# Kernel optimization log

Hardware: AMD Instinct MI355X
Metric: run time of the kernel (lower is better)

The kernel has to match this reference:

```python
import jax, jax.numpy as jnp
import numpy as np
from jax import lax

N_NEURONS = 128
BATCH = 2048
SEQ = 128
INFTY = 1e8


def setup_inputs() -> dict:
    key = jax.random.key(0)
    ks = jax.random.split(key, 10)
    n = N_NEURONS
    lim = 1.0 / np.sqrt(n)  # torch LSTMCell default init scale
    return {
        "enc_outputs": jax.random.normal(ks[0], (BATCH, SEQ, n), jnp.float32),
        "h0": jax.random.normal(ks[1], (BATCH, n), jnp.float32),
        "c0": jax.random.normal(ks[2], (BATCH, n), jnp.float32),
        "dec_first_input": jnp.zeros((1, n), jnp.float32),
        "W_ref": jax.random.normal(ks[3], (1, n, n), jnp.float32),
        "W_out": jax.random.normal(ks[4], (n, n), jnp.float32),
        "v": jax.random.normal(ks[5], (n,), jnp.float32),
        "W_ih": jax.random.uniform(ks[6], (4 * n, n), jnp.float32, -lim, lim),
        "W_hh": jax.random.uniform(ks[7], (4 * n, n), jnp.float32, -lim, lim),
        "b_ih": jax.random.uniform(ks[8], (4 * n,), jnp.float32, -lim, lim),
        "b_hh": jax.random.uniform(ks[9], (4 * n,), jnp.float32, -lim, lim),
    }


def _decode(enc_outputs, h0, c0, dec_first_input, W_ref, W_out, v, W_ih, W_hh, b_ih, b_hh):
    B, S, n = enc_outputs.shape
    # step-invariant pointer projection of encoder outputs (the conv1d term)
    enc_term = jnp.einsum("bsn,mn->bsm", enc_outputs, W_ref[0])  # [B,S,n]
    batch_idx = jnp.arange(B)
    keys = jax.random.split(jax.random.key(1234), S)
    inp0 = jnp.broadcast_to(dec_first_input, (B, n))
    mask0 = jnp.zeros((B, S), enc_outputs.dtype)

    def step(carry, key):
        h, c, mask, inp = carry
        # LSTMCell: gate order i, f, g, o (torch convention)
        gates = inp @ W_ih.T + b_ih + h @ W_hh.T + b_hh  # [B,4n]
        i_g, f_g, g_g, o_g = jnp.split(gates, 4, axis=1)
        c = jax.nn.sigmoid(f_g) * c + jax.nn.sigmoid(i_g) * jnp.tanh(g_g)
        h = jax.nn.sigmoid(o_g) * jnp.tanh(c)
        # pointer attention scores
        dec_term = (h @ W_out)[:, None, :]  # [B,1,n]
        scores = jnp.sum(v * jnp.tanh(enc_term + dec_term), axis=-1)  # [B,S]
        masked = scores - INFTY * mask
        loc = jax.random.categorical(key, masked)  # [B] int, non-differentiable sample
        logp = jnp.take_along_axis(jax.nn.log_softmax(masked, axis=1), loc[:, None], axis=1)[:, 0]
        mask = mask.at[batch_idx, loc].set(1.0)
        inp = enc_outputs[batch_idx, loc, :]  # gather next decoder input
        return (h, c, mask, inp), (loc, logp)

    _, (locs, logps) = lax.scan(step, (h0, c0, mask0, inp0), keys)
    locs = locs.T  # [B,S]
    tour = jnp.concatenate([locs, locs[:, :1]], axis=1)  # append first location
    log_prob = jnp.sum(logps, axis=0)  # [B]
    return log_prob, tour


def reference(enc_outputs, h0, c0, dec_first_input, W_ref, W_out, v, W_ih, W_hh, b_ih, b_hh):
    return _decode(enc_outputs, h0, c0, dec_first_input, W_ref, W_out, v, W_ih, W_hh, b_ih, b_hh)
```

## Files before the change

### kernel.cpp

```cpp
#include <hip/hip_runtime.h>
#include <cstdint>
#include <cstddef>

#pragma clang fp contract(off)

#define PRNG_PARTITIONABLE 1

#define INFTY_F 1.0e8f
#define TINY_F 1.17549435e-38f

__device__ __forceinline__ float fdiv_rn(float n, float q) {
  float y0 = __builtin_amdgcn_rcpf(q);
  float y  = fmaf(fmaf(-q, y0, 1.0f), y0, y0);
  float r0 = n * y;
  float e0 = fmaf(-q, r0, n);
  float r1 = fmaf(e0, y, r0);
  float e1 = fmaf(-q, r1, n);
  return fmaf(e1, y, r1);
}

__device__ __forceinline__ void tf2x32(uint32_t k0, uint32_t k1, uint32_t x0, uint32_t x1,
                                       uint32_t& o0, uint32_t& o1) {
  uint32_t ks2 = k0 ^ k1 ^ 0x1BD11BDAu;
  uint32_t v0 = x0 + k0, v1 = x1 + k1;
#define TF_R(r) { v0 += v1; v1 = (v1 << (r)) | (v1 >> (32 - (r))); v1 ^= v0; }
  TF_R(13) TF_R(15) TF_R(26) TF_R(6)
  v0 += k1;  v1 += ks2 + 1u;
  TF_R(17) TF_R(29) TF_R(16) TF_R(24)
  v0 += ks2; v1 += k0 + 2u;
  TF_R(13) TF_R(15) TF_R(26) TF_R(6)
  v0 += k0;  v1 += k1 + 3u;
  TF_R(17) TF_R(29) TF_R(16) TF_R(24)
  v0 += k1;  v1 += ks2 + 4u;
  TF_R(13) TF_R(15) TF_R(26) TF_R(6)
  v0 += ks2; v1 += k0 + 5u;
#undef TF_R
  o0 = v0; o1 = v1;
}

__device__ __forceinline__ uint32_t random_bits32(uint32_t k0, uint32_t k1, uint32_t j) {
#if PRNG_PARTITIONABLE
  uint32_t o0, o1;
  tf2x32(k0, k1, 0u, j, o0, o1);
  return o0 ^ o1;
#else
  uint32_t o0, o1;
  if (j < 131072u) { tf2x32(k0, k1, j, j + 131072u, o0, o1); return o0; }
  else             { tf2x32(k0, k1, j - 131072u, j, o0, o1); return o1; }
#endif
}

__device__ __forceinline__ float xla_tanhf(float x) {
  float xc = fminf(fmaxf(x, -9.0f), 9.0f);
  float x2 = xc * xc;
  float p = -2.76076847742355e-16f;
  p = (p * x2) + 2.00018790482477e-13f;
  p = (p * x2) + -8.60467152213735e-11f;
  p = (p * x2) + 5.12229709037114e-08f;
  p = (p * x2) + 1.48572235717979e-05f;
  p = (p * x2) + 6.37261928875436e-04f;
  p = (p * x2) + 4.89352455891786e-03f;
  float num = xc * p;
  float q = 1.19825839466702e-06f;
  q = (q * x2) + 1.18534705686654e-04f;
  q = (q * x2) + 2.26843463243900e-03f;
  q = (q * x2) + 4.89352518554385e-03f;
  float r = fdiv_rn(num, q);
  return (fabsf(x) < 0.0004f) ? x : r;
}

__device__ __forceinline__ void xla_tanh2(float xa, float xb, float& ra, float& rb) {
  float xca = fminf(fmaxf(xa, -9.0f), 9.0f);
  float xcb = fminf(fmaxf(xb, -9.0f), 9.0f);
  float x2a = xca * xca, x2b = xcb * xcb;
  float pa = -2.76076847742355e-16f, pb = -2.76076847742355e-16f;
  pa = (pa * x2a) + 2.00018790482477e-13f;  pb = (pb * x2b) + 2.00018790482477e-13f;
  pa = (pa * x2a) + -8.60467152213735e-11f; pb = (pb * x2b) + -8.60467152213735e-11f;
  pa = (pa * x2a) + 5.12229709037114e-08f;  pb = (pb * x2b) + 5.12229709037114e-08f;
  pa = (pa * x2a) + 1.48572235717979e-05f;  pb = (pb * x2b) + 1.48572235717979e-05f;
  pa = (pa * x2a) + 6.37261928875436e-04f;  pb = (pb * x2b) + 6.37261928875436e-04f;
  pa = (pa * x2a) + 4.89352455891786e-03f;  pb = (pb * x2b) + 4.89352455891786e-03f;
  float na = xca * pa, nb = xcb * pb;
  float qa = 1.19825839466702e-06f, qb = 1.19825839466702e-06f;
  qa = (qa * x2a) + 1.18534705686654e-04f; qb = (qb * x2b) + 1.18534705686654e-04f;
  qa = (qa * x2a) + 2.26843463243900e-03f; qb = (qb * x2b) + 2.26843463243900e-03f;
  qa = (qa * x2a) + 4.89352518554385e-03f; qb = (qb * x2b) + 4.89352518554385e-03f;
  float da = fdiv_rn(na, qa), db = fdiv_rn(nb, qb);
  ra = (fabsf(xa) < 0.0004f) ? xa : da;
  rb = (fabsf(xb) < 0.0004f) ? xb : db;
}

__device__ __forceinline__ float xla_expf(float x) {
  x = fminf(x, 88.3762626647950f);
  x = fmaxf(x, -88.3762626647949f);
  float m = floorf((x * 1.44269504088896341f) + 0.5f);
  float r = x - (m * 0.693359375f);
  r = r - (m * -2.12194440e-4f);
  float r2 = r * r;
  float y = 1.9875691500E-4f;
  y = (y * r) + 1.3981999507E-3f;
  y = (y * r) + 8.3334519073E-3f;
  y = (y * r) + 4.1665795894E-2f;
  y = (y * r) + 1.6666665459E-1f;
  y = (y * r) + 5.0000001201E-1f;
  y = (y * r2) + r;
  y = y + 1.0f;
  int mi = (int)m;
  float s = __uint_as_float((uint32_t)((mi + 127) << 23));
  return y * s;
}

__device__ __forceinline__ float xla_sigmoidf(float x) {
  return 1.0f / (1.0f + xla_expf(-x));
}

__device__ __forceinline__ float xla_logf(float x) {
  uint32_t b = __float_as_uint(x);
  float e = (float)((int)(b >> 23) - 126);
  float m = __uint_as_float((b & 0x007fffffu) | 0x3f000000u);
  bool mlt = (m < 0.707106781186547524f);
  float tmp = mlt ? m : 0.0f;
  e = e - (mlt ? 1.0f : 0.0f);
  float xx = (m - 1.0f) + tmp;
  float z = xx * xx;
  float y = 7.0376836292E-2f;
  y = (y * xx) + -1.1514610310E-1f;
  y = (y * xx) + 1.1676998740E-1f;
  y = (y * xx) + -1.2420140846E-1f;
  y = (y * xx) + 1.4249322787E-1f;
  y = (y * xx) + -1.6668057665E-1f;
  y = (y * xx) + 2.0000714765E-1f;
  y = (y * xx) + -2.4999993993E-1f;
  y = (y * xx) + 3.3333331174E-1f;
  y = y * xx;
  y = y * z;
  y = y + (e * -2.12194440e-4f);
  y = y - (z * 0.5f);
  float res = xx + y;
  res = res + (e * 0.693359375f);
  return res;
}

__device__ __forceinline__ float gumbel_from_bits(uint32_t bits) {
  float f = __uint_as_float((bits >> 9) | 0x3f800000u) - 1.0f;
  float u = (f * 1.0f) + TINY_F;
  u = fmaxf(TINY_F, u);
  return -xla_logf(-xla_logf(u));
}

__global__ void k_keys(uint32_t* __restrict__ keys) {
  int t = threadIdx.x;
  if (t >= 128) return;
#if PRNG_PARTITIONABLE
  uint32_t o0, o1;
  tf2x32(0u, 1234u, 0u, (uint32_t)t, o0, o1);
  keys[2 * t] = o0; keys[2 * t + 1] = o1;
#else
  uint32_t o0, o1, a, bb;
  if (t < 64) {
    tf2x32(0u, 1234u, (uint32_t)(2 * t),     (uint32_t)(128 + 2 * t), o0, o1); a  = o0;
    tf2x32(0u, 1234u, (uint32_t)(2 * t + 1), (uint32_t)(129 + 2 * t), o0, o1); bb = o0;
  } else {
    tf2x32(0u, 1234u, (uint32_t)(2 * t - 128), (uint32_t)(2 * t),     o0, o1); a  = o1;
    tf2x32(0u, 1234u, (uint32_t)(2 * t - 127), (uint32_t)(2 * t + 1), o0, o1); bb = o1;
  }
  keys[2 * t] = a; keys[2 * t + 1] = bb;
#endif
}

__global__ void k_trans(const float* __restrict__ Wih, const float* __restrict__ Whh,
                        float* __restrict__ WihT, float* __restrict__ WhhT) {
  int idx = blockIdx.x * blockDim.x + threadIdx.x;
  if (idx < 65536) {
    int r = idx >> 7, k = idx & 127;
    WihT[k * 512 + r] = Wih[idx];
    WhhT[k * 512 + r] = Whh[idx];
  }
}

__global__ __launch_bounds__(128) void k_encT(const float* __restrict__ enc,
                                              const float* __restrict__ Wref,
                                              float* __restrict__ encT) {
  __shared__ float el[64 * 132];
  __shared__ float ot[64 * 129];
  int tid = threadIdx.x;
  int b  = blockIdx.x >> 1;
  int sh = blockIdx.x & 1;
  const float* eb = enc + (size_t)b * 16384 + (size_t)sh * 8192;
  for (int i = tid; i < 8192; i += 128) {
    int s = i >> 7, n = i & 127;
    el[s * 132 + n] = eb[i];
  }
  __syncthreads();
  int sl = tid & 63;
  int mh = tid >> 6;
  for (int ml = 0; ml < 64; ++ml) {
    int m = mh * 64 + ml;
    const float4* wr = (const float4*)(Wref + m * 128);
    float acc = 0.0f;
#pragma unroll 8
    for (int q = 0; q < 32; ++q) {
      float4 w4 = wr[q];
      float4 e4 = *(const float4*)&el[sl * 132 + 4 * q];
      acc = fmaf(e4.x, w4.x, acc); acc = fmaf(e4.y, w4.y, acc);
      acc = fmaf(e4.z, w4.z, acc); acc = fmaf(e4.w, w4.w, acc);
    }
    ot[sl * 129 + m] = acc;
  }
  __syncthreads();
  float* op = encT + (size_t)b * 16384 + (size_t)(sh * 64) * 128;
  for (int i = tid; i < 8192; i += 128)
    op[i] = ot[(i >> 7) * 129 + (i & 127)];
}

__global__ __launch_bounds__(512, 4) void k_main(
    const float* __restrict__ enc, const float* __restrict__ h0,
    const float* __restrict__ c0, const float* __restrict__ dec_first,
    const float* __restrict__ W_out, const float* __restrict__ v,
    const float* __restrict__ b_ih, const float* __restrict__ b_hh,
    const float* __restrict__ WihT, const float* __restrict__ WhhT,
    const float* __restrict__ encT, const uint32_t* __restrict__ keys,
    float* __restrict__ out) {
  __shared__ float xI_s[128][8];
  __shared__ float c_s[4][128];
  __shared__ float gates_s[4][512];
  __shared__ float2 vdec2_s[4][128];
  __shared__ float bih_s[512];
  __shared__ float bhh_s[512];
  __shared__ float v_s[128];
  __shared__ uint32_t keys_s[256];
  __shared__ int cu_s[4][128];
  __shared__ int pos_s[4][128];
  __shared__ float val_s[512];
  __shared__ float msk_s[512];
  __shared__ int   sc_s[512];
  __shared__ int   loc_s[4];

  const int tid  = threadIdx.x;
  const int lane = tid & 63;
  const int w    = tid >> 6;
  const int g4   = w >> 1;
  const int half = w & 1;
  const int s4   = half * 64 + lane;
  const int bbase = blockIdx.x * 4;
  const int b4   = bbase + g4;

  bih_s[tid] = b_ih[tid];
  bhh_s[tid] = b_hh[tid];
  if (tid < 256) keys_s[tid] = keys[tid];
  if (tid < 128) v_s[tid] = v[tid];
  {
    int g = tid >> 7, j = tid & 127;
    xI_s[j][g]     = dec_first[j];
    xI_s[j][4 + g] = h0[(size_t)(bbase + g) * 128 + j];
    c_s[g][j] = c0[(size_t)(bbase + g) * 128 + j];
    cu_s[g][j] = j;
    pos_s[g][j] = j;
  }
  float logp_sum = 0.0f;
  float* tour = out + 2048;
  __syncthreads();

  for (int step = 0; step < 128; ++step) {
    {
      const int r = tid;
      float aA0 = 0.0f, aA1 = 0.0f, aA2 = 0.0f, aA3 = 0.0f;
      float aB0 = 0.0f, aB1 = 0.0f, aB2 = 0.0f, aB3 = 0.0f;
      const float* pih = WihT + r;
      const float* phh = WhhT + r;
#pragma unroll 8
      for (int k = 0; k < 128; ++k) {
        float4 xi = *(const float4*)&xI_s[k][0];
        float4 xh = *(const float4*)&xI_s[k][4];
        float wih = pih[k * 512], whh = phh[k * 512];
        aA0 = fmaf(xi.x, wih, aA0);
        aA1 = fmaf(xi.y, wih, aA1);
        aA2 = fmaf(xi.z, wih, aA2);
        aA3 = fmaf(xi.w, wih, aA3);
        aB0 = fmaf(xh.x, whh, aB0);
        aB1 = fmaf(xh.y, whh, aB1);
        aB2 = fmaf(xh.z, whh, aB2);
        aB3 = fmaf(xh.w, whh, aB3);
      }
      float b1 = bih_s[r], b2 = bhh_s[r];
      gates_s[0][r] = (((aA0 + b1) + aB0) + b2);
      gates_s[1][r] = (((aA1 + b1) + aB1) + b2);
      gates_s[2][r] = (((aA2 + b1) + aB2) + b2);
      gates_s[3][r] = (((aA3 + b1) + aB3) + b2);
    }
    __syncthreads();

    {
      int g = tid >> 7, j = tid & 127;
      float gi = gates_s[g][j], gf = gates_s[g][128 + j];
      float gg = gates_s[g][256 + j], go = gates_s[g][384 + j];
      float si = xla_sigmoidf(gi), sf = xla_sigmoidf(gf), so = xla_sigmoidf(go);
      float gt = xla_tanhf(gg);
      float cold = c_s[g][j];
      float cn = (sf * cold) + (si * gt);
      c_s[g][j] = cn;
      xI_s[j][4 + g] = so * xla_tanhf(cn);
    }
    __syncthreads();

    {
      int g = tid >> 7, m = tid & 127;
      float acc = 0.0f;
      const float* wo = W_out + m;
#pragma unroll 8
      for (int k = 0; k < 128; ++k)
        acc = fmaf(xI_s[k][4 + g], wo[k * 128], acc);
      vdec2_s[g][m] = make_float2(v_s[m], acc);
    }
    __syncthreads();

    const int u = 128 - step;
    {
      const int q = tid;
      float masked = -INFTY_F, val = -INFTY_F;
      int sc = 0x7fffffff;
      if (q < 4 * u) {
        int bq = (q >= u) + (q >= 2 * u) + (q >= 3 * u);
        int e  = q - bq * u;
        sc = cu_s[bq][e];
        const int bb = bbase + bq;
        uint32_t kk0 = keys_s[2 * step], kk1 = keys_s[2 * step + 1];
        uint32_t j0 = (uint32_t)bb * 128u + (uint32_t)sc;
        float gmb = gumbel_from_bits(random_bits32(kk0, kk1, j0));
        const float* ep = encT + ((size_t)bb * 128 + (size_t)sc) * 128;
        float acc = 0.0f;
#pragma unroll 8
        for (int m4 = 0; m4 < 32; ++m4) {
          float4 e4 = *(const float4*)&ep[4 * m4];
          float4 vd01 = *(const float4*)&vdec2_s[bq][4 * m4];
          float4 vd23 = *(const float4*)&vdec2_s[bq][4 * m4 + 2];
          float t0, t1, t2, t3;
          xla_tanh2(e4.x + vd01.y, e4.y + vd01.w, t0, t1);
          xla_tanh2(e4.z + vd23.y, e4.w + vd23.w, t2, t3);
          acc = acc + (vd01.x * t0);
          acc = acc + (vd01.z * t1);
          acc = acc + (vd23.x * t2);
          acc = acc + (vd23.z * t3);
        }
        masked = acc;
        val = gmb + masked;
      }
      val_s[q] = val;
      msk_s[q] = masked;
      sc_s[q]  = sc;
    }
    __syncthreads();

    if (w < 4) {
      const int g = w;
      const int base = g * u;
      float vaA = -INFTY_F, mkA = -INFTY_F;
      float vaB = -INFTY_F, mkB = -INFTY_F;
      int iaA = 0x7fffffff, iaB = 0x7fffffff;
      if (lane < u)      { vaA = val_s[base + lane];      iaA = sc_s[base + lane];      mkA = msk_s[base + lane]; }
      if (lane + 64 < u) { vaB = val_s[base + lane + 64]; iaB = sc_s[base + lane + 64]; mkB = msk_s[base + lane + 64]; }
      float va = vaA; int ia = iaA;
      if (vaB > va || (vaB == va && iaB < ia)) { va = vaB; ia = iaB; }
      float mx = fmaxf(mkA, mkB);
      float se = 0.0f;
#pragma unroll
      for (int off = 32; off > 0; off >>= 1) {
        float vo = __shfl_xor(va, off, 64);
        int io = __shfl_xor(ia, off, 64);
        if (vo > va || (vo == va && io < ia)) { va = vo; ia = io; }
        mx = fmaxf(mx, __shfl_xor(mx, off, 64));
      }
      if (lane < u)      se = se + expf(mkA - mx);
      if (lane + 64 < u) se = se + expf(mkB - mx);
#pragma unroll
      for (int off = 32; off > 0; off >>= 1) se = se + __shfl_xor(se, off, 64);
      const int loc = ia;
      int p = pos_s[g][loc];
      float msel = msk_s[base + p];
      if (lane == 0) {
        loc_s[g] = loc;
        tour[(size_t)(bbase + g) * 129 + step] = (float)loc;
        if (step == 0) tour[(size_t)(bbase + g) * 129 + 128] = (float)loc;
        int last = cu_s[g][u - 1];
        cu_s[g][p] = last;
        pos_s[g][last] = p;
      }
      float lse = logf(se);
      logp_sum = logp_sum + ((msel - mx) - lse);
    }
    __syncthreads();

    {
      const int loc = loc_s[g4];
      const float* er = enc + (size_t)b4 * 16384 + (size_t)loc * 128;
      xI_s[s4][g4] = er[s4];
    }
    __syncthreads();
  }

  if (w < 4 && lane == 0) out[bbase + w] = logp_sum;
}

extern "C" void kernel_launch(void* const* d_in, const int* in_sizes, int n_in,
                              void* d_out, int out_size, void* d_ws, size_t ws_size,
                              hipStream_t stream) {
  (void)in_sizes; (void)n_in; (void)out_size;
  const float* enc       = (const float*)d_in[0];
  const float* h0        = (const float*)d_in[1];
  const float* c0        = (const float*)d_in[2];
  const float* dec_first = (const float*)d_in[3];
  const float* W_ref     = (const float*)d_in[4];
  const float* W_out     = (const float*)d_in[5];
  const float* v         = (const float*)d_in[6];
  const float* W_ih      = (const float*)d_in[7];
  const float* W_hh      = (const float*)d_in[8];
  const float* b_ih      = (const float*)d_in[9];
  const float* b_hh      = (const float*)d_in[10];

  const size_t encT_elems = (size_t)2048 * 16384;
  size_t need = (encT_elems + 65536 + 65536) * sizeof(float) + 256 * sizeof(uint32_t);
  if (ws_size < need) return;

  float* encT = (float*)d_ws;
  float* WihT = encT + encT_elems;
  float* WhhT = WihT + 65536;
  uint32_t* keys = (uint32_t*)(WhhT + 65536);
  float* out = (float*)d_out;

  k_keys<<<dim3(1), dim3(128), 0, stream>>>(keys);
  k_trans<<<dim3(256), dim3(256), 0, stream>>>(W_ih, W_hh, WihT, WhhT);
  k_encT<<<dim3(4096), dim3(128), 0, stream>>>(enc, W_ref, encT);
  k_main<<<dim3(512), dim3(512), 0, stream>>>(enc, h0, c0, dec_first, W_out, v,
                                              b_ih, b_hh, WihT, WhhT, encT, keys, out);
}
```

Before: 5.762 ms.

## Overlap next-step recurrent matvec with attention scoring on idle waves

```diff
diff --git a/kernel.cpp b/kernel.cpp
--- a/kernel.cpp
+++ b/kernel.cpp
@@ -225,6 +225,7 @@
   __shared__ float c_s[4][128];
   __shared__ float gates_s[4][512];
   __shared__ float2 vdec2_s[4][128];
+  __shared__ __align__(16) float aB_s[512][4];
   __shared__ float bih_s[512];
   __shared__ float bhh_s[512];
   __shared__ float v_s[128];
@@ -262,7 +263,7 @@
   __syncthreads();
 
   for (int step = 0; step < 128; ++step) {
-    {
+    if (step < 17) {
       const int r = tid;
       float aA0 = 0.0f, aA1 = 0.0f, aA2 = 0.0f, aA3 = 0.0f;
       float aB0 = 0.0f, aB1 = 0.0f, aB2 = 0.0f, aB3 = 0.0f;
@@ -287,6 +288,25 @@
       gates_s[1][r] = (((aA1 + b1) + aB1) + b2);
       gates_s[2][r] = (((aA2 + b1) + aB2) + b2);
       gates_s[3][r] = (((aA3 + b1) + aB3) + b2);
+    } else {
+      const int r = tid;
+      float aA0 = 0.0f, aA1 = 0.0f, aA2 = 0.0f, aA3 = 0.0f;
+      const float* pih = WihT + r;
+#pragma unroll 8
+      for (int k = 0; k < 128; ++k) {
+        float4 xi = *(const float4*)&xI_s[k][0];
+        float wih = pih[k * 512];
+        aA0 = fmaf(xi.x, wih, aA0);
+        aA1 = fmaf(xi.y, wih, aA1);
+        aA2 = fmaf(xi.z, wih, aA2);
+        aA3 = fmaf(xi.w, wih, aA3);
+      }
+      float b1 = bih_s[r], b2 = bhh_s[r];
+      float4 aB = *(const float4*)&aB_s[r][0];
+      gates_s[0][r] = (((aA0 + b1) + aB.x) + b2);
+      gates_s[1][r] = (((aA1 + b1) + aB.y) + b2);
+      gates_s[2][r] = (((aA2 + b1) + aB.z) + b2);
+      gates_s[3][r] = (((aA3 + b1) + aB.w) + b2);
     }
     __syncthreads();
 
@@ -315,39 +335,51 @@
     __syncthreads();
 
     const int u = 128 - step;
-    {
+    const int nact = (4 * u + 63) >> 6;
+    if (tid < 4 * u) {
       const int q = tid;
-      float masked = -INFTY_F, val = -INFTY_F;
-      int sc = 0x7fffffff;
-      if (q < 4 * u) {
-        int bq = (q >= u) + (q >= 2 * u) + (q >= 3 * u);
-        int e  = q - bq * u;
-        sc = cu_s[bq][e];
-        const int bb = bbase + bq;
-        uint32_t kk0 = keys_s[2 * step], kk1 = keys_s[2 * step + 1];
-        uint32_t j0 = (uint32_t)bb * 128u + (uint32_t)sc;
-        float gmb = gumbel_from_bits(random_bits32(kk0, kk1, j0));
-        const float* ep = encT + ((size_t)bb * 128 + (size_t)sc) * 128;
-        float acc = 0.0f;
+      int bq = (q >= u) + (q >= 2 * u) + (q >= 3 * u);
+      int e  = q - bq * u;
+      int sc = cu_s[bq][e];
+      const int bb = bbase + bq;
+      uint32_t kk0 = keys_s[2 * step], kk1 = keys_s[2 * step + 1];
+      uint32_t j0 = (uint32_t)bb * 128u + (uint32_t)sc;
+      float gmb = gumbel_from_bits(random_bits32(kk0, kk1, j0));
+      const float* ep = encT + ((size_t)bb * 128 + (size_t)sc) * 128;
+      float acc = 0.0f;
 #pragma unroll 8
-        for (int m4 = 0; m4 < 32; ++m4) {
-          float4 e4 = *(const float4*)&ep[4 * m4];
-          float4 vd01 = *(const float4*)&vdec2_s[bq][4 * m4];
-          float4 vd23 = *(const float4*)&vdec2_s[bq][4 * m4 + 2];
-          float t0, t1, t2, t3;
-          xla_tanh2(e4.x + vd01.y, e4.y + vd01.w, t0, t1);
-          xla_tanh2(e4.z + vd23.y, e4.w + vd23.w, t2, t3);
-          acc = acc + (vd01.x * t0);
-          acc = acc + (vd01.z * t1);
-          acc = acc + (vd23.x * t2);
-          acc = acc + (vd23.z * t3);
+      for (int m4 = 0; m4 < 32; ++m4) {
+        float4 e4 = *(const float4*)&ep[4 * m4];
+        float4 vd01 = *(const float4*)&vdec2_s[bq][4 * m4];
+        float4 vd23 = *(const float4*)&vdec2_s[bq][4 * m4 + 2];
+        float t0, t1, t2, t3;
+        xla_tanh2(e4.x + vd01.y, e4.y + vd01.w, t0, t1);
+        xla_tanh2(e4.z + vd23.y, e4.w + vd23.w, t2, t3);
+        acc = acc + (vd01.x * t0);
+        acc = acc + (vd01.z * t1);
+        acc = acc + (vd23.x * t2);
+        acc = acc + (vd23.z * t3);
+      }
+      val_s[q] = gmb + acc;
+      msk_s[q] = acc;
+      sc_s[q]  = sc;
+    } else if (w >= nact && step >= 16 && step < 127) {
+      const int nfree = 8 - nact;
+      for (int r = (w - nact) * 64 + lane; r < 512; r += nfree * 64) {
+        float a0 = 0.0f, a1 = 0.0f, a2 = 0.0f, a3 = 0.0f;
+        const float* phh = WhhT + r;
+#pragma unroll 4
+        for (int k = 0; k < 128; ++k) {
+          float4 xh = *(const float4*)&xI_s[k][4];
+          float whh = phh[k * 512];
+          a0 = fmaf(xh.x, whh, a0);
+          a1 = fmaf(xh.y, whh, a1);
+          a2 = fmaf(xh.z, whh, a2);
+          a3 = fmaf(xh.w, whh, a3);
         }
-        masked = acc;
-        val = gmb + masked;
-      }
-      val_s[q] = val;
-      msk_s[q] = masked;
-      sc_s[q]  = sc;
+        float4 o; o.x = a0; o.y = a1; o.z = a2; o.w = a3;
+        *(float4*)&aB_s[r][0] = o;
+      }
     }
     __syncthreads();
 
```

New measurement: 6.422 ms. 1.11x slower.
